# Performance work log

Hardware: AMD Instinct MI355X
Metric: run time of the kernel (lower is better)

Reference implementation:

```python
import jax, jax.numpy as jnp
import numpy as np

B, S, C = 4, 8192, 256        # batch, seq len, channels
NW, WS, PSZ, D = 2048, 256, 256, 32  # words, word_size, p_size, window radius


def setup_inputs() -> dict:
    key = jax.random.key(0)
    k0, k1, k2, k3, k4 = jax.random.split(key, 5)
    q = jax.random.normal(k0, (B, S, C), jnp.float32)
    c_t = jax.random.normal(k1, (B, NW, WS), jnp.float32)
    # scale weights ~1/sqrt(fan_in) so sigmoid in predictive alignment is not saturated
    W_a = jax.random.normal(k2, (WS, C), jnp.float32) / np.sqrt(C).astype(np.float32)
    W_p = jax.random.normal(k3, (PSZ, WS), jnp.float32) / np.sqrt(WS).astype(np.float32)
    V_p = jax.random.normal(k4, (1, PSZ), jnp.float32) / np.sqrt(PSZ).astype(np.float32)
    return {"q": q, "c_t": c_t, "W_a": W_a, "W_p": W_p, "V_p": V_p}


def reference(q, c_t, W_a, W_p, V_p):
    Bq, Sq, Cq = q.shape
    # predictive alignment: p_t = S * sigmoid(V_p(tanh(W_p(c_t))))  -> [B, NW, 1]
    p_t = Sq * jax.nn.sigmoid(jnp.tanh(c_t @ W_p.T) @ V_p.T)
    # window positions s in [p-D, p+D]; torch .long() truncates (p_t > 0 so == floor)
    offs = jnp.arange(-D, D + 1)                       # [K]
    s = p_t[..., 0].astype(jnp.int32)[:, :, None] + offs  # [B, NW, K]
    # pad a leading NaN row; out-of-range indices map to it (clamp then mod)
    q_pad = jnp.concatenate([jnp.full((Bq, 1, Cq), jnp.nan, q.dtype), q], axis=1)  # [B, S+1, C]
    idx = jnp.clip(s + 1, 0, Sq + 1) % (Sq + 1)        # S+1 wraps to the NaN row (0)
    qw = jax.vmap(lambda qb, ib: qb[ib])(q_pad, idx)   # [B, NW, K, C] gathered windows
    nan_mask = jnp.isnan(qw[..., 0])                   # [B, NW, K]
    qw = jnp.where(nan_mask[..., None], 0.0, qw)       # zero invalid keys (used for output too)
    Wq = qw @ W_a.T                                    # [B, NW, K, WS]
    a_t = jnp.einsum('bwkd,bwd->bwk', Wq, c_t)         # per-window scores
    a_t = jnp.where(nan_mask, -jnp.inf, a_t)           # NaN keys -> -inf before softmax
    prob = jax.nn.softmax(a_t, axis=2)
    # Gaussian truncation around predicted position p_t
    prob = prob * jnp.exp(-2.0 * jnp.square((s.astype(q.dtype) - p_t) / D))
    out = jnp.einsum('bwk,bwkc->bwc', prob, qw)        # [B, NW, C]
    return out
```

## Files before the change

kernel.cpp:

```cpp
#include <hip/hip_runtime.h>
#include <math.h>

#define BB 4
#define S 8192
#define C 256
#define NW 2048
#define WS 256
#define PSZ 256
#define DD 32
#define KK 65
#define TOTW (BB * NW)

#define KC 64
#define LDA 68
#define NBKT 64
#define TBKT (BB * NBKT)

__global__ __launch_bounds__(256) void prep_B(const float* __restrict__ Wp,
                                              const float* __restrict__ Wa,
                                              float* __restrict__ Bp) {
    const int k = blockIdx.x;
    const int t = threadIdx.x;
    Bp[k * 512 + t] = Wp[t * WS + k];
    Bp[k * 512 + 256 + t] = Wa[k * C + t];
}

__global__ __launch_bounds__(256, 4) void precomp_gemm(const float* __restrict__ ct,
                                                       const float* __restrict__ Bp,
                                                       const float* __restrict__ Vp,
                                                       float* __restrict__ ptpart,
                                                       float* __restrict__ g) {
    __shared__ __align__(16) float Al[KC][LDA];
    __shared__ __align__(16) float Bl[KC][LDA];

    const int t = threadIdx.x;
    const int bm = blockIdx.x >> 3;
    const int bn = blockIdx.x & 7;
    const int tm = t >> 4;
    const int tn = t & 15;
    const int sm = t >> 2;
    const int sf = t & 3;

    const float4* ct4 = (const float4*)ct;
    const float4* B4  = (const float4*)Bp;

    float acc[4][4] = {{0.f}};

    for (int kc = 0; kc < 256; kc += KC) {
        __syncthreads();
#pragma unroll
        for (int i = 0; i < 4; i++) {
            const float4 a = ct4[(size_t)(bm * 64 + sm) * 64 + (kc >> 2) + sf + i * 4];
            const int kl = (sf + i * 4) * 4;
            Al[kl + 0][sm] = a.x;
            Al[kl + 1][sm] = a.y;
            Al[kl + 2][sm] = a.z;
            Al[kl + 3][sm] = a.w;
        }
#pragma unroll
        for (int i = 0; i < 4; i++) {
            const float4 b = B4[(size_t)(kc + sm) * 128 + bn * 16 + sf + i * 4];
            *(float4*)&Bl[sm][(sf + i * 4) * 4] = b;
        }
        __syncthreads();

#pragma unroll 8
        for (int kk = 0; kk < KC; kk++) {
            const float4 a = *(const float4*)&Al[kk][tm * 4];
            const float4 b = *(const float4*)&Bl[kk][tn * 4];
            acc[0][0] = fmaf(a.x, b.x, acc[0][0]);
            acc[0][1] = fmaf(a.x, b.y, acc[0][1]);
            acc[0][2] = fmaf(a.x, b.z, acc[0][2]);
            acc[0][3] = fmaf(a.x, b.w, acc[0][3]);
            acc[1][0] = fmaf(a.y, b.x, acc[1][0]);
            acc[1][1] = fmaf(a.y, b.y, acc[1][1]);
            acc[1][2] = fmaf(a.y, b.z, acc[1][2]);
            acc[1][3] = fmaf(a.y, b.w, acc[1][3]);
            acc[2][0] = fmaf(a.z, b.x, acc[2][0]);
            acc[2][1] = fmaf(a.z, b.y, acc[2][1]);
            acc[2][2] = fmaf(a.z, b.z, acc[2][2]);
            acc[2][3] = fmaf(a.z, b.w, acc[2][3]);
            acc[3][0] = fmaf(a.w, b.x, acc[3][0]);
            acc[3][1] = fmaf(a.w, b.y, acc[3][1]);
            acc[3][2] = fmaf(a.w, b.z, acc[3][2]);
            acc[3][3] = fmaf(a.w, b.w, acc[3][3]);
        }
    }

    if (bn >= 4) {
        const int col = bn * 64 + tn * 4 - 256;
#pragma unroll
        for (int i = 0; i < 4; i++) {
            const int row = bm * 64 + tm * 4 + i;
            *(float4*)&g[(size_t)row * 256 + col] =
                make_float4(acc[i][0], acc[i][1], acc[i][2], acc[i][3]);
        }
    } else {
        const float4 vp4 = ((const float4*)Vp)[bn * 16 + tn];
#pragma unroll
        for (int i = 0; i < 4; i++) {
            float v = tanhf(acc[i][0]) * vp4.x;
            v = fmaf(tanhf(acc[i][1]), vp4.y, v);
            v = fmaf(tanhf(acc[i][2]), vp4.z, v);
            v = fmaf(tanhf(acc[i][3]), vp4.w, v);
#pragma unroll
            for (int off = 8; off >= 1; off >>= 1) v += __shfl_xor(v, off);
            if (tn == 0) {
                const int row = bm * 64 + tm * 4 + i;
                ptpart[row * 4 + bn] = v;
            }
        }
    }
}

__global__ __launch_bounds__(256) void sort_all(const float* __restrict__ ptpart,
                                                float* __restrict__ pt,
                                                int* __restrict__ perm) {
    __shared__ int hist[TBKT];
    __shared__ int scan[TBKT];

    const int t = threadIdx.x;
    hist[t] = 0;
    __syncthreads();

    int bkt[32];
#pragma unroll
    for (int it = 0; it < 32; it++) {
        const int wg = it * 256 + t;
        const float4 pp = ((const float4*)ptpart)[wg];
        const float x = (pp.x + pp.y) + (pp.z + pp.w);
        const float p = (float)S / (1.f + expf(-x));
        pt[wg] = p;
        const int s0 = (int)p;
        bkt[it] = (wg >> 11) * NBKT + min(NBKT - 1, max(0, s0 >> 7));
        atomicAdd(&hist[bkt[it]], 1);
    }
    __syncthreads();

    int v = hist[t];
    scan[t] = v;
    __syncthreads();
    for (int d = 1; d < TBKT; d <<= 1) {
        const int x = (t >= d) ? scan[t - d] : 0;
        __syncthreads();
        scan[t] += x;
        __syncthreads();
    }
    hist[t] = scan[t] - v;
    __syncthreads();

#pragma unroll
    for (int it = 0; it < 32; it++) {
        const int wg = it * 256 + t;
        const int pos = atomicAdd(&hist[bkt[it]], 1);
        perm[pos] = wg;
    }
}

__global__ __launch_bounds__(256) void attn(const float* __restrict__ q,
                                            const float* __restrict__ g,
                                            const float* __restrict__ pt,
                                            const int* __restrict__ perm,
                                            float* __restrict__ out) {
    __shared__ __align__(16) float4 pbuf[16][68];
    __shared__ float mbuf[4], dbuf[4];

    const int tid = threadIdx.x;
    const int l = tid & 63;
    const int wv = tid >> 6;
    const int sub = l & 15;
    const int kslot = tid >> 4;

    const int bid = blockIdx.x;
    const int sb = (bid & 7) * 1024 + (bid >> 3);
    const int wg = perm[sb];
    const int b = wg >> 11;

    const float p = pt[wg];
    const int s0 = (int)p;

    const float* grow = g + (size_t)wg * C + sub * 4;
    const float4 g0 = *(const float4*)(grow);
    const float4 g1 = *(const float4*)(grow + 64);
    const float4 g2 = *(const float4*)(grow + 128);
    const float4 g3 = *(const float4*)(grow + 192);

    const float* qb = q + (size_t)b * S * C + sub * 4;

    float e[5];
#pragma unroll
    for (int it = 0; it < 5; it++) {
        const int k = it * 16 + kslot;
        const int s = s0 + k - DD;
        const bool valid = (k <= 64) && ((unsigned)s < (unsigned)S);
        const float* qr = qb + (size_t)min(max(s, 0), S - 1) * C;
        const float4 q0 = *(const float4*)(qr);
        const float4 q1 = *(const float4*)(qr + 64);
        const float4 q2 = *(const float4*)(qr + 128);
        const float4 q3 = *(const float4*)(qr + 192);
        float d0 = q0.x * g0.x, d1 = q1.x * g1.x, d2 = q2.x * g2.x, d3 = q3.x * g3.x;
        d0 = fmaf(q0.y, g0.y, d0); d1 = fmaf(q1.y, g1.y, d1);
        d2 = fmaf(q2.y, g2.y, d2); d3 = fmaf(q3.y, g3.y, d3);
        d0 = fmaf(q0.z, g0.z, d0); d1 = fmaf(q1.z, g1.z, d1);
        d2 = fmaf(q2.z, g2.z, d2); d3 = fmaf(q3.z, g3.z, d3);
        d0 = fmaf(q0.w, g0.w, d0); d1 = fmaf(q1.w, g1.w, d1);
        d2 = fmaf(q2.w, g2.w, d2); d3 = fmaf(q3.w, g3.w, d3);
        float d = (d0 + d1) + (d2 + d3);
#pragma unroll
        for (int off = 8; off >= 1; off >>= 1) d += __shfl_xor(d, off);
        e[it] = valid ? d : -3e38f;
    }

    float m = e[0];
#pragma unroll
    for (int it = 1; it < 5; it++) m = fmaxf(m, e[it]);
    m = fmaxf(m, __shfl_xor(m, 16));
    m = fmaxf(m, __shfl_xor(m, 32));
    if (l == 0) mbuf[wv] = m;
    __syncthreads();
    const float M = fmaxf(fmaxf(mbuf[0], mbuf[1]), fmaxf(mbuf[2], mbuf[3]));

    float den = 0.f;
#pragma unroll
    for (int it = 0; it < 5; it++) {
        e[it] = __expf(e[it] - M);
        den += e[it];
    }
    den += __shfl_xor(den, 16);
    den += __shfl_xor(den, 32);
    if (l == 0) dbuf[wv] = den;

#pragma unroll
    for (int it = 0; it < 5; it++) {
        const float fs = (float)(s0 + it * 16 + kslot - DD) - p;
        const float tt = fs * (1.f / (float)DD);
        e[it] *= __expf(-2.f * tt * tt);
    }

    float4 a0 = {0,0,0,0}, a1 = {0,0,0,0}, a2 = {0,0,0,0}, a3 = {0,0,0,0};
#pragma unroll
    for (int it = 0; it < 5; it++) {
        const int s = s0 + it * 16 + kslot - DD;
        const float* qr = qb + (size_t)min(max(s, 0), S - 1) * C;
        const float4 q0 = *(const float4*)(qr);
        const float4 q1 = *(const float4*)(qr + 64);
        const float4 q2 = *(const float4*)(qr + 128);
        const float4 q3 = *(const float4*)(qr + 192);
        const float w = e[it];
        a0.x = fmaf(w, q0.x, a0.x); a0.y = fmaf(w, q0.y, a0.y);
        a0.z = fmaf(w, q0.z, a0.z); a0.w = fmaf(w, q0.w, a0.w);
        a1.x = fmaf(w, q1.x, a1.x); a1.y = fmaf(w, q1.y, a1.y);
        a1.z = fmaf(w, q1.z, a1.z); a1.w = fmaf(w, q1.w, a1.w);
        a2.x = fmaf(w, q2.x, a2.x); a2.y = fmaf(w, q2.y, a2.y);
        a2.z = fmaf(w, q2.z, a2.z); a2.w = fmaf(w, q2.w, a2.w);
        a3.x = fmaf(w, q3.x, a3.x); a3.y = fmaf(w, q3.y, a3.y);
        a3.z = fmaf(w, q3.z, a3.z); a3.w = fmaf(w, q3.w, a3.w);
    }

    pbuf[kslot][0 * 17 + sub] = a0;
    pbuf[kslot][1 * 17 + sub] = a1;
    pbuf[kslot][2 * 17 + sub] = a2;
    pbuf[kslot][3 * 17 + sub] = a3;
    __syncthreads();

    if (tid < 64) {
        const float dtot = dbuf[0] + dbuf[1] + dbuf[2] + dbuf[3];
        const int j = tid >> 4, sb2 = tid & 15;
        float4 s0v = {0,0,0,0};
#pragma unroll
        for (int ks = 0; ks < 16; ks++) {
            const float4 v = pbuf[ks][j * 17 + sb2];
            s0v.x += v.x; s0v.y += v.y; s0v.z += v.z; s0v.w += v.w;
        }
        const float r = 1.f / dtot;
        s0v.x *= r; s0v.y *= r; s0v.z *= r; s0v.w *= r;
        *(float4*)(out + (size_t)wg * C + tid * 4) = s0v;
    }
}

extern "C" void kernel_launch(void* const* d_in, const int* in_sizes, int n_in,
                              void* d_out, int out_size, void* d_ws, size_t ws_size,
                              hipStream_t stream) {
    const float* q  = (const float*)d_in[0];
    const float* ct = (const float*)d_in[1];
    const float* Wa = (const float*)d_in[2];
    const float* Wp = (const float*)d_in[3];
    const float* Vp = (const float*)d_in[4];
    float* out = (float*)d_out;

    char* ws = (char*)d_ws;
    float* Bp     = (float*)ws;
    float* ptpart = (float*)(ws + 524288);
    float* pt     = (float*)(ws + 655360);
    int*   perm   = (int*)  (ws + 688128);
    float* g      = (float*)(ws + 720896);

    prep_B<<<256, 256, 0, stream>>>(Wp, Wa, Bp);
    precomp_gemm<<<1024, 256, 0, stream>>>(ct, Bp, Vp, ptpart, g);
    sort_all<<<1, 256, 0, stream>>>(ptpart, pt, perm);
    attn<<<TOTW, 256, 0, stream>>>(q, g, pt, perm, out);
}
```

Measured before the change: 103.5 us.

## Process two windows per block with per-wave softmax and shuffle merge

The attention kernel now handles two sorted windows per block and launches half as many blocks. Each wave keeps its own softmax max and denominator, reduces its partial output with cross-lane shuffles instead of a 16-slot shared buffer, and the partial results are rescaled and combined in a final flash-style merge. This drops one barrier before the exponentials and shrinks shared-memory traffic, and a block can prefetch the second window's g row early. In exchange the two windows run one after the other in a block, and there are extra shuffles and exp rescales.

```diff
diff --git a/kernel.cpp b/kernel.cpp
--- a/kernel.cpp
+++ b/kernel.cpp
@@ -162,120 +162,148 @@
                                             const float* __restrict__ pt,
                                             const int* __restrict__ perm,
                                             float* __restrict__ out) {
-    __shared__ __align__(16) float4 pbuf[16][68];
+    __shared__ __align__(16) float4 accbuf[4][64];
     __shared__ float mbuf[4], dbuf[4];
 
     const int tid = threadIdx.x;
     const int l = tid & 63;
     const int wv = tid >> 6;
+    const int gw = l >> 4;
     const int sub = l & 15;
     const int kslot = tid >> 4;
 
     const int bid = blockIdx.x;
-    const int sb = (bid & 7) * 1024 + (bid >> 3);
-    const int wg = perm[sb];
-    const int b = wg >> 11;
-
-    const float p = pt[wg];
-    const int s0 = (int)p;
-
-    const float* grow = g + (size_t)wg * C + sub * 4;
-    const float4 g0 = *(const float4*)(grow);
-    const float4 g1 = *(const float4*)(grow + 64);
-    const float4 g2 = *(const float4*)(grow + 128);
-    const float4 g3 = *(const float4*)(grow + 192);
-
-    const float* qb = q + (size_t)b * S * C + sub * 4;
-
-    float e[5];
-#pragma unroll
-    for (int it = 0; it < 5; it++) {
-        const int k = it * 16 + kslot;
-        const int s = s0 + k - DD;
-        const bool valid = (k <= 64) && ((unsigned)s < (unsigned)S);
-        const float* qr = qb + (size_t)min(max(s, 0), S - 1) * C;
-        const float4 q0 = *(const float4*)(qr);
-        const float4 q1 = *(const float4*)(qr + 64);
-        const float4 q2 = *(const float4*)(qr + 128);
-        const float4 q3 = *(const float4*)(qr + 192);
-        float d0 = q0.x * g0.x, d1 = q1.x * g1.x, d2 = q2.x * g2.x, d3 = q3.x * g3.x;
-        d0 = fmaf(q0.y, g0.y, d0); d1 = fmaf(q1.y, g1.y, d1);
-        d2 = fmaf(q2.y, g2.y, d2); d3 = fmaf(q3.y, g3.y, d3);
-        d0 = fmaf(q0.z, g0.z, d0); d1 = fmaf(q1.z, g1.z, d1);
-        d2 = fmaf(q2.z, g2.z, d2); d3 = fmaf(q3.z, g3.z, d3);
-        d0 = fmaf(q0.w, g0.w, d0); d1 = fmaf(q1.w, g1.w, d1);
-        d2 = fmaf(q2.w, g2.w, d2); d3 = fmaf(q3.w, g3.w, d3);
-        float d = (d0 + d1) + (d2 + d3);
-#pragma unroll
-        for (int off = 8; off >= 1; off >>= 1) d += __shfl_xor(d, off);
-        e[it] = valid ? d : -3e38f;
-    }
-
-    float m = e[0];
-#pragma unroll
-    for (int it = 1; it < 5; it++) m = fmaxf(m, e[it]);
-    m = fmaxf(m, __shfl_xor(m, 16));
-    m = fmaxf(m, __shfl_xor(m, 32));
-    if (l == 0) mbuf[wv] = m;
-    __syncthreads();
-    const float M = fmaxf(fmaxf(mbuf[0], mbuf[1]), fmaxf(mbuf[2], mbuf[3]));
-
-    float den = 0.f;
-#pragma unroll
-    for (int it = 0; it < 5; it++) {
-        e[it] = __expf(e[it] - M);
-        den += e[it];
-    }
-    den += __shfl_xor(den, 16);
-    den += __shfl_xor(den, 32);
-    if (l == 0) dbuf[wv] = den;
-
-#pragma unroll
-    for (int it = 0; it < 5; it++) {
-        const float fs = (float)(s0 + it * 16 + kslot - DD) - p;
-        const float tt = fs * (1.f / (float)DD);
-        e[it] *= __expf(-2.f * tt * tt);
-    }
-
-    float4 a0 = {0,0,0,0}, a1 = {0,0,0,0}, a2 = {0,0,0,0}, a3 = {0,0,0,0};
-#pragma unroll
-    for (int it = 0; it < 5; it++) {
-        const int s = s0 + it * 16 + kslot - DD;
-        const float* qr = qb + (size_t)min(max(s, 0), S - 1) * C;
-        const float4 q0 = *(const float4*)(qr);
-        const float4 q1 = *(const float4*)(qr + 64);
-        const float4 q2 = *(const float4*)(qr + 128);
-        const float4 q3 = *(const float4*)(qr + 192);
-        const float w = e[it];
-        a0.x = fmaf(w, q0.x, a0.x); a0.y = fmaf(w, q0.y, a0.y);
-        a0.z = fmaf(w, q0.z, a0.z); a0.w = fmaf(w, q0.w, a0.w);
-        a1.x = fmaf(w, q1.x, a1.x); a1.y = fmaf(w, q1.y, a1.y);
-        a1.z = fmaf(w, q1.z, a1.z); a1.w = fmaf(w, q1.w, a1.w);
-        a2.x = fmaf(w, q2.x, a2.x); a2.y = fmaf(w, q2.y, a2.y);
-        a2.z = fmaf(w, q2.z, a2.z); a2.w = fmaf(w, q2.w, a2.w);
-        a3.x = fmaf(w, q3.x, a3.x); a3.y = fmaf(w, q3.y, a3.y);
-        a3.z = fmaf(w, q3.z, a3.z); a3.w = fmaf(w, q3.w, a3.w);
-    }
-
-    pbuf[kslot][0 * 17 + sub] = a0;
-    pbuf[kslot][1 * 17 + sub] = a1;
-    pbuf[kslot][2 * 17 + sub] = a2;
-    pbuf[kslot][3 * 17 + sub] = a3;
-    __syncthreads();
-
-    if (tid < 64) {
-        const float dtot = dbuf[0] + dbuf[1] + dbuf[2] + dbuf[3];
-        const int j = tid >> 4, sb2 = tid & 15;
-        float4 s0v = {0,0,0,0};
-#pragma unroll
-        for (int ks = 0; ks < 16; ks++) {
-            const float4 v = pbuf[ks][j * 17 + sb2];
-            s0v.x += v.x; s0v.y += v.y; s0v.z += v.z; s0v.w += v.w;
-        }
-        const float r = 1.f / dtot;
-        s0v.x *= r; s0v.y *= r; s0v.z *= r; s0v.w *= r;
-        *(float4*)(out + (size_t)wg * C + tid * 4) = s0v;
-    }
+    const int sbase = (bid & 7) * 512 + (bid >> 3);
+    const int wg1 = perm[2 * sbase];
+    const int wg2 = perm[2 * sbase + 1];
+    const float p1 = pt[wg1];
+    const float p2 = pt[wg2];
+    const int s01 = (int)p1;
+    const int s02 = (int)p2;
+
+    const float* g1row = g + (size_t)wg1 * C + sub * 4;
+    const float4 G10 = *(const float4*)(g1row);
+    const float4 G11 = *(const float4*)(g1row + 64);
+    const float4 G12 = *(const float4*)(g1row + 128);
+    const float4 G13 = *(const float4*)(g1row + 192);
+    const float* g2row = g + (size_t)wg2 * C + sub * 4;
+    const float4 G20 = *(const float4*)(g2row);
+    const float4 G21 = *(const float4*)(g2row + 64);
+    const float4 G22 = *(const float4*)(g2row + 128);
+    const float4 G23 = *(const float4*)(g2row + 192);
+
+    const float* qb1 = q + (size_t)(wg1 >> 11) * S * C + sub * 4;
+    const float* qb2 = q + (size_t)(wg2 >> 11) * S * C + sub * 4;
+
+    auto process = [&](int wg, float p, int s0, const float* qb,
+                       const float4& g0, const float4& g1,
+                       const float4& g2, const float4& g3) {
+        float e[5];
+#pragma unroll
+        for (int it = 0; it < 5; it++) {
+            const int k = it * 16 + kslot;
+            const int s = s0 + k - DD;
+            const bool valid = (k <= 64) && ((unsigned)s < (unsigned)S);
+            const float* qr = qb + (size_t)min(max(s, 0), S - 1) * C;
+            const float4 q0 = *(const float4*)(qr);
+            const float4 q1 = *(const float4*)(qr + 64);
+            const float4 q2 = *(const float4*)(qr + 128);
+            const float4 q3 = *(const float4*)(qr + 192);
+            float d0 = q0.x * g0.x, d1 = q1.x * g1.x;
+            float d2 = q2.x * g2.x, d3 = q3.x * g3.x;
+            d0 = fmaf(q0.y, g0.y, d0); d1 = fmaf(q1.y, g1.y, d1);
+            d2 = fmaf(q2.y, g2.y, d2); d3 = fmaf(q3.y, g3.y, d3);
+            d0 = fmaf(q0.z, g0.z, d0); d1 = fmaf(q1.z, g1.z, d1);
+            d2 = fmaf(q2.z, g2.z, d2); d3 = fmaf(q3.z, g3.z, d3);
+            d0 = fmaf(q0.w, g0.w, d0); d1 = fmaf(q1.w, g1.w, d1);
+            d2 = fmaf(q2.w, g2.w, d2); d3 = fmaf(q3.w, g3.w, d3);
+            float d = (d0 + d1) + (d2 + d3);
+#pragma unroll
+            for (int off = 8; off >= 1; off >>= 1) d += __shfl_xor(d, off);
+            e[it] = valid ? d : -3e38f;
+        }
+
+        float m = e[0];
+#pragma unroll
+        for (int it = 1; it < 5; it++) m = fmaxf(m, e[it]);
+        m = fmaxf(m, __shfl_xor(m, 16));
+        m = fmaxf(m, __shfl_xor(m, 32));
+
+        float den = 0.f;
+#pragma unroll
+        for (int it = 0; it < 5; it++) {
+            e[it] = __expf(e[it] - m);
+            den += e[it];
+        }
+        den += __shfl_xor(den, 16);
+        den += __shfl_xor(den, 32);
+
+#pragma unroll
+        for (int it = 0; it < 5; it++) {
+            const float fs = (float)(s0 + it * 16 + kslot - DD) - p;
+            const float tt = fs * (1.f / (float)DD);
+            e[it] *= __expf(-2.f * tt * tt);
+        }
+
+        float4 a0 = {0,0,0,0}, a1 = {0,0,0,0}, a2 = {0,0,0,0}, a3 = {0,0,0,0};
+#pragma unroll
+        for (int it = 0; it < 5; it++) {
+            const int s = s0 + it * 16 + kslot - DD;
+            const float* qr = qb + (size_t)min(max(s, 0), S - 1) * C;
+            const float4 q0 = *(const float4*)(qr);
+            const float4 q1 = *(const float4*)(qr + 64);
+            const float4 q2 = *(const float4*)(qr + 128);
+            const float4 q3 = *(const float4*)(qr + 192);
+            const float w = e[it];
+            a0.x = fmaf(w, q0.x, a0.x); a0.y = fmaf(w, q0.y, a0.y);
+            a0.z = fmaf(w, q0.z, a0.z); a0.w = fmaf(w, q0.w, a0.w);
+            a1.x = fmaf(w, q1.x, a1.x); a1.y = fmaf(w, q1.y, a1.y);
+            a1.z = fmaf(w, q1.z, a1.z); a1.w = fmaf(w, q1.w, a1.w);
+            a2.x = fmaf(w, q2.x, a2.x); a2.y = fmaf(w, q2.y, a2.y);
+            a2.z = fmaf(w, q2.z, a2.z); a2.w = fmaf(w, q2.w, a2.w);
+            a3.x = fmaf(w, q3.x, a3.x); a3.y = fmaf(w, q3.y, a3.y);
+            a3.z = fmaf(w, q3.z, a3.z); a3.w = fmaf(w, q3.w, a3.w);
+        }
+
+#define MERGE(v) { v += __shfl_xor(v, 16); v += __shfl_xor(v, 32); }
+        MERGE(a0.x) MERGE(a0.y) MERGE(a0.z) MERGE(a0.w)
+        MERGE(a1.x) MERGE(a1.y) MERGE(a1.z) MERGE(a1.w)
+        MERGE(a2.x) MERGE(a2.y) MERGE(a2.z) MERGE(a2.w)
+        MERGE(a3.x) MERGE(a3.y) MERGE(a3.z) MERGE(a3.w)
+#undef MERGE
+
+        float4 o = a0;
+        if (gw == 1) o = a1;
+        else if (gw == 2) o = a2;
+        else if (gw == 3) o = a3;
+        accbuf[wv][l] = o;
+        if (l == 0) { mbuf[wv] = m; dbuf[wv] = den; }
+        __syncthreads();
+
+        if (tid < 64) {
+            const float M = fmaxf(fmaxf(mbuf[0], mbuf[1]), fmaxf(mbuf[2], mbuf[3]));
+            const float sc0 = __expf(mbuf[0] - M);
+            const float sc1 = __expf(mbuf[1] - M);
+            const float sc2 = __expf(mbuf[2] - M);
+            const float sc3 = __expf(mbuf[3] - M);
+            const float dtot = dbuf[0]*sc0 + dbuf[1]*sc1 + dbuf[2]*sc2 + dbuf[3]*sc3;
+            const float4 v0 = accbuf[0][tid];
+            const float4 v1 = accbuf[1][tid];
+            const float4 v2 = accbuf[2][tid];
+            const float4 v3 = accbuf[3][tid];
+            const float r = 1.f / dtot;
+            float4 oo;
+            oo.x = (v0.x*sc0 + v1.x*sc1 + v2.x*sc2 + v3.x*sc3) * r;
+            oo.y = (v0.y*sc0 + v1.y*sc1 + v2.y*sc2 + v3.y*sc3) * r;
+            oo.z = (v0.z*sc0 + v1.z*sc1 + v2.z*sc2 + v3.z*sc3) * r;
+            oo.w = (v0.w*sc0 + v1.w*sc1 + v2.w*sc2 + v3.w*sc3) * r;
+            *(float4*)(out + (size_t)wg * C + tid * 4) = oo;
+        }
+    };
+
+    process(wg1, p1, s01, qb1, G10, G11, G12, G13);
+    __syncthreads();
+    process(wg2, p2, s02, qb2, G20, G21, G22, G23);
 }
 
 extern "C" void kernel_launch(void* const* d_in, const int* in_sizes, int n_in,
@@ -298,5 +326,5 @@
     prep_B<<<256, 256, 0, stream>>>(Wp, Wa, Bp);
     precomp_gemm<<<1024, 256, 0, stream>>>(ct, Bp, Vp, ptpart, g);
     sort_all<<<1, 256, 0, stream>>>(ptpart, pt, perm);
-    attn<<<TOTW, 256, 0, stream>>>(q, g, pt, perm, out);
-}
+    attn<<<TOTW / 2, 256, 0, stream>>>(q, g, pt, perm, out);
+}
```

Result: no change. 104.7 us (+1.2%).
